# Optimization experiments

Hardware: AMD Instinct MI355X
Metric: run time of the kernel (lower is better)

The kernel has to match this reference:

```python
import jax, jax.numpy as jnp
import numpy as np

H = 128          # image resolution (matches init_kwargs H)
B = 2            # batch (matches init_kwargs B)
F = 1024         # number of triangle faces
PI = 3.141592653589793


def setup_inputs() -> dict:
    key = jax.random.key(0)
    # vertices in NDC [-1, 1]: [B, faces, 3 verts, xyz]
    v = jax.random.uniform(key, (B, F, 3, 3), dtype=jnp.float32, minval=-1.0, maxval=1.0)
    return {"v_tensor": v, "C": 16}


def _render(tmp, C):
    # tmp: [B,F,3,3] with (x,y) already in pixel coords, z in [-1,1].
    # Counting-sort rasterization expressed in closed form: instead of sorting
    # per-pixel ray/mesh intersections into in/out intervals, we use the signed
    # (winding-number) formulation: occupancy f(zt) = sum_i s_i * H(zt - zt_i)
    # where s_i = +1 for front faces, -1 for back faces. The cosine (FOF)
    # coefficients then reduce to a sum over intersections -- fully vectorized.
    x = tmp[..., 0]  # [B,F,3]
    y = tmp[..., 1]
    z = tmp[..., 2]
    px = jnp.arange(H, dtype=tmp.dtype)[None, :]   # pixel-center x, [1,H]
    py = jnp.arange(H, dtype=tmp.dtype)[:, None]   # pixel-center y, [H,1]

    def vert(i):
        return x[..., i, None, None], y[..., i, None, None], z[..., i, None, None]

    x0, y0, z0 = vert(0)
    x1, y1, z1 = vert(1)
    x2, y2, z2 = vert(2)

    # edge functions -> barycentric numerators, each [B,F,H,H]
    e0 = (x2 - x1) * (py - y1) - (y2 - y1) * (px - x1)
    e1 = (x0 - x2) * (py - y2) - (y0 - y2) * (px - x2)
    e2 = (x1 - x0) * (py - y0) - (y1 - y0) * (px - x0)
    area = (x1 - x0) * (y2 - y0) - (x2 - x0) * (y1 - y0)  # [B,F,1,1]

    nz = area != 0
    inv = jnp.where(nz, 1.0 / jnp.where(nz, area, 1.0), 0.0)
    l0, l1, l2 = e0 * inv, e1 * inv, e2 * inv
    inside = (l0 >= 0) & (l1 >= 0) & (l2 >= 0) & nz
    s = jnp.sign(area)                      # front/back facing sign
    w = jnp.where(inside, s, jnp.zeros((), tmp.dtype))  # [B,F,H,H]

    # interpolated depth, remapped to zt in [0,1]
    zt = jnp.clip((l0 * z0 + l1 * z1 + l2 * z2 + 1.0) * 0.5, 0.0, 1.0)

    # Fourier occupancy coefficients over zt in [0,1]:
    #   c0 = int f dzt           = sum_i s_i * (1 - zt_i)
    #   ck = 2 int f cos(k pi zt) dzt = -2/(k pi) * sum_i s_i * sin(k pi zt_i)
    coeffs = [jnp.sum(w * (1.0 - zt), axis=1)]            # [B,H,H]
    for k in range(1, C):
        coeffs.append(jnp.sum(w * jnp.sin((k * PI) * zt), axis=1) * (-2.0 / (k * PI)))
    return jnp.stack(coeffs, axis=1)  # [B,C,H,H]


def reference(v_tensor, C):
    a = jnp.array([H / 2.0, -H / 2.0, 1.0], dtype=v_tensor.dtype)
    b = jnp.array([H / 2.0 - 0.5, H / 2.0 - 0.5, 0.0], dtype=v_tensor.dtype)
    tmp = v_tensor * a + b  # affine transform from the torch forward
    return _render(tmp, C)
```

## Files before the change

### kernel.cpp

```cpp
#include <hip/hip_runtime.h>
#include <math.h>

#define HH 128
#define BB 2
#define FF 1024
#define CC 16
#define PIF 3.14159265358979323846f
#define RS 14

__global__ __launch_bounds__(256) void fof_setup(const float* __restrict__ v,
                                                 double* __restrict__ rec,
                                                 int* __restrict__ bbox) {
#pragma clang fp contract(off)
    int idx = blockIdx.x * 256 + threadIdx.x;
    if (idx >= BB * FF) return;
    const float* vp = v + (size_t)idx * 9;

    double X0 = fma((double)vp[0],  64.0, 63.5);
    double Y0 = fma((double)vp[1], -64.0, 63.5);
    double Z0 = (double)vp[2];
    double X1 = fma((double)vp[3],  64.0, 63.5);
    double Y1 = fma((double)vp[4], -64.0, 63.5);
    double Z1 = (double)vp[5];
    double X2 = fma((double)vp[6],  64.0, 63.5);
    double Y2 = fma((double)vp[7], -64.0, 63.5);
    double Z2 = (double)vp[8];

    double d0x = X2 - X1, d0y = Y2 - Y1;
    double d1x = X0 - X2, d1y = Y0 - Y2;
    double d2x = X1 - X0, d2y = Y1 - Y0;
    double area = d1x * d2y - d1y * d2x;
    double inv  = (area != 0.0) ? 1.0 / area : 0.0;
    double sg   = (area > 0.0) ? 1.0 : ((area < 0.0) ? -1.0 : 0.0);

    double A0 = d0x * inv, B0 = -d0y * inv, C0 = (d0y * X1 - d0x * Y1) * inv;
    double A1 = d1x * inv, B1 = -d1y * inv, C1 = (d1y * X2 - d1x * Y2) * inv;
    double A2 = d2x * inv, B2 = -d2y * inv, C2 = (d2y * X0 - d2x * Y0) * inv;

    double ZA = (A0 * Z0 + A1 * Z1 + A2 * Z2) * 0.5;
    double ZB = (B0 * Z0 + B1 * Z1 + B2 * Z2) * 0.5;
    double ZC = (C0 * Z0 + C1 * Z1 + C2 * Z2 + 1.0) * 0.5;

    double* r = rec + (size_t)idx * RS;
    r[0] = A0; r[1] = B0; r[2] = C0;
    r[3] = A1; r[4] = B1; r[5] = C1;
    r[6] = A2; r[7] = B2; r[8] = C2;
    r[9] = sg; r[10] = ZA; r[11] = ZB; r[12] = ZC; r[13] = 0.0;

    float x0 = (float)X0, y0 = (float)Y0;
    float x1 = (float)X1, y1 = (float)Y1;
    float x2 = (float)X2, y2 = (float)Y2;
    float xmn = fminf(x0, fminf(x1, x2)) - 0.5f;
    float xmx = fmaxf(x0, fmaxf(x1, x2)) + 0.5f;
    float ymn = fminf(y0, fminf(y1, y2)) - 0.5f;
    float ymx = fmaxf(y0, fmaxf(y1, y2)) + 0.5f;
    int txmin = (int)ceilf((xmn - 7.f) * 0.125f);
    int txmax = (int)floorf(xmx * 0.125f);
    int tymin = (int)ceilf((ymn - 7.f) * 0.125f);
    int tymax = (int)floorf(ymx * 0.125f);
    txmin = max(0, min(15, txmin)); txmax = max(0, min(15, txmax));
    tymin = max(0, min(15, tymin)); tymax = max(0, min(15, tymax));
    bbox[idx] = (sg == 0.0) ? (1 | (0 << 8) | (1 << 16) | (0 << 24))
                            : (txmin | (txmax << 8) | (tymin << 16) | (tymax << 24));
}

__global__ __launch_bounds__(512) void fof_main(const double* __restrict__ rec,
                                                const int* __restrict__ bbox,
                                                float* __restrict__ part) {
    __shared__ float S1[4][64][17];
    __shared__ float S2[2][64][17];
    __shared__ float S3[64][17];

    int blk  = blockIdx.x;
    int b    = blk >> 9;
    int rest = blk & 511;
    int half = rest >> 8;
    int tile = rest & 255;
    int ty   = tile >> 4;
    int tx   = tile & 15;
    int wv   = __builtin_amdgcn_readfirstlane((int)(threadIdx.x >> 6));
    int lane = threadIdx.x & 63;

    double pxd = (double)(tx * 8 + (lane & 7));
    double pyd = (double)(ty * 8 + (lane >> 3));

    float acc[CC];
#pragma unroll
    for (int k = 0; k < CC; ++k) acc[k] = 0.f;

    int gfb = b * FF + half * 512 + wv * 64;

    int pk = bbox[gfb + lane];
    int txmin = pk & 255, txmax = (pk >> 8) & 255;
    int tymin = (pk >> 16) & 255, tymax = (pk >> 24) & 255;
    bool pass = !((tx < txmin) | (tx > txmax) | (ty < tymin) | (ty > tymax));
    unsigned long long m = __ballot(pass);

    const double* rp = rec + (size_t)gfb * RS;
    while (m) {
        int j = __builtin_ctzll(m);
        m &= m - 1;
        j = __builtin_amdgcn_readfirstlane(j);
        const double* r = rp + j * RS;

        double l0 = fma(r[0], pyd, fma(r[1], pxd, r[2]));
        double l1 = fma(r[3], pyd, fma(r[4], pxd, r[5]));
        double l2 = fma(r[6], pyd, fma(r[7], pxd, r[8]));
        bool inside = (l0 >= 0.0) & (l1 >= 0.0) & (l2 >= 0.0);

        if (__any(inside)) {
            double u = fma(r[10], pyd, fma(r[11], pxd, r[12]));
            u = fmin(fmax(u, 0.0), 1.0);
            float zt = (float)u;
            float w  = inside ? (float)r[9] : 0.f;

            float t = PIF * zt;
            float s1, c1;
            __sincosf(t, &s1, &c1);
            acc[0] = fmaf(w, 1.f - zt, acc[0]);
            acc[1] = fmaf(w, s1, acc[1]);
            float twoc = c1 + c1;
            float skm2 = 0.f, skm1 = s1;
#pragma unroll
            for (int k = 2; k < CC; ++k) {
                float sk = fmaf(twoc, skm1, -skm2);
                acc[k] = fmaf(w, sk, acc[k]);
                skm2 = skm1;
                skm1 = sk;
            }
        }
    }

    if (wv >= 4) {
#pragma unroll
        for (int k = 0; k < CC; ++k) S1[wv - 4][lane][k] = acc[k];
    }
    __syncthreads();
    if (wv < 4) {
#pragma unroll
        for (int k = 0; k < CC; ++k) acc[k] += S1[wv][lane][k];
    }
    if (wv == 2 || wv == 3) {
#pragma unroll
        for (int k = 0; k < CC; ++k) S2[wv - 2][lane][k] = acc[k];
    }
    __syncthreads();
    if (wv < 2) {
#pragma unroll
        for (int k = 0; k < CC; ++k) acc[k] += S2[wv][lane][k];
    }
    if (wv == 1) {
#pragma unroll
        for (int k = 0; k < CC; ++k) S3[lane][k] = acc[k];
    }
    __syncthreads();
    if (wv == 0) {
        int xo = tx * 8 + (lane & 7);
        int yo = ty * 8 + (lane >> 3);
#pragma unroll
        for (int k = 0; k < CC; ++k) {
            part[(((b * 2 + half) * CC + k) * (HH * HH)) + yo * HH + xo] =
                acc[k] + S3[lane][k];
        }
    }
}

__global__ __launch_bounds__(256) void fof_combine(const float4* __restrict__ part4,
                                                   float4* __restrict__ out4) {
    int i   = blockIdx.x * 256 + threadIdx.x;
    int b   = i >> 16;
    int rem = i & 65535;
    int k   = rem >> 12;
    int r   = rem & 4095;
    float4 p0 = part4[(b * 32 + k) * 4096 + r];
    float4 p1 = part4[(b * 32 + 16 + k) * 4096 + r];
    float scale = (k == 0) ? 1.f : (-2.f / (PIF * (float)k));
    float4 o;
    o.x = (p0.x + p1.x) * scale;
    o.y = (p0.y + p1.y) * scale;
    o.z = (p0.z + p1.z) * scale;
    o.w = (p0.w + p1.w) * scale;
    out4[(b * 16 + k) * 4096 + r] = o;
}

extern "C" void kernel_launch(void* const* d_in, const int* in_sizes, int n_in,
                              void* d_out, int out_size, void* d_ws, size_t ws_size,
                              hipStream_t stream) {
    const float* v = (const float*)d_in[0];
    float* out = (float*)d_out;

    double* rec  = (double*)d_ws;
    int*    bbox = (int*)((char*)d_ws + 229376);
    float*  part = (float*)((char*)d_ws + 237568);

    fof_setup<<<(BB * FF + 255) / 256, 256, 0, stream>>>(v, rec, bbox);
    fof_main<<<BB * 2 * 256, 512, 0, stream>>>(rec, bbox, part);
    fof_combine<<<512, 256, 0, stream>>>((const float4*)part, (float4*)out);
}
```

Before: 85.61 us.

## Use fp32 edge tests with fp64 fallback, packed sin recurrence, drop combine kernel

The inner rasterization loop now evaluates edge functions and depth in fp32, with a per-face error bound. It falls back to the fp64 coefficients only when some lane's edge value lies within that bound, so the fp64 work is kept off the hot path. The sin harmonics use hardware v_sin/v_cos in revolution units and a two-wide packed Chebyshev recurrence. Each block now covers all 1024 faces with 1024 threads, which removes the half split and the separate combine kernel, at the cost of half as many blocks and a deeper shared-memory reduction.

```diff
diff --git a/kernel.cpp b/kernel.cpp
--- a/kernel.cpp
+++ b/kernel.cpp
@@ -6,12 +6,13 @@
 #define FF 1024
 #define CC 16
 #define PIF 3.14159265358979323846f
-#define RS 14
+
+typedef float f2 __attribute__((ext_vector_type(2)));
 
 __global__ __launch_bounds__(256) void fof_setup(const float* __restrict__ v,
-                                                 double* __restrict__ rec,
+                                                 float* __restrict__ recf,
+                                                 double* __restrict__ recd,
                                                  int* __restrict__ bbox) {
-#pragma clang fp contract(off)
     int idx = blockIdx.x * 256 + threadIdx.x;
     if (idx >= BB * FF) return;
     const float* vp = v + (size_t)idx * 9;
@@ -41,11 +42,22 @@
     double ZB = (B0 * Z0 + B1 * Z1 + B2 * Z2) * 0.5;
     double ZC = (C0 * Z0 + C1 * Z1 + C2 * Z2 + 1.0) * 0.5;
 
-    double* r = rec + (size_t)idx * RS;
-    r[0] = A0; r[1] = B0; r[2] = C0;
-    r[3] = A1; r[4] = B1; r[5] = C1;
-    r[6] = A2; r[7] = B2; r[8] = C2;
-    r[9] = sg; r[10] = ZA; r[11] = ZB; r[12] = ZC; r[13] = 0.0;
+    double M0 = (fabs(A0) + fabs(B0)) * 135.0 + fabs(C0);
+    double M1 = (fabs(A1) + fabs(B1)) * 135.0 + fabs(C1);
+    double M2 = (fabs(A2) + fabs(B2)) * 135.0 + fabs(C2);
+    float eps = (float)(1e-6 * fmax(M0, fmax(M1, M2)));
+
+    float* rf = recf + (size_t)idx * 16;
+    rf[0] = (float)A0; rf[1] = (float)B0; rf[2] = (float)C0;
+    rf[3] = (float)A1; rf[4] = (float)B1; rf[5] = (float)C1;
+    rf[6] = (float)A2; rf[7] = (float)B2; rf[8] = (float)C2;
+    rf[9] = (float)ZA; rf[10] = (float)ZB; rf[11] = (float)ZC;
+    rf[12] = (float)sg; rf[13] = eps; rf[14] = 0.f; rf[15] = 0.f;
+
+    double* rd = recd + (size_t)idx * 10;
+    rd[0] = A0; rd[1] = B0; rd[2] = C0;
+    rd[3] = A1; rd[4] = B1; rd[5] = C1;
+    rd[6] = A2; rd[7] = B2; rd[8] = C2; rd[9] = 0.0;
 
     float x0 = (float)X0, y0 = (float)Y0;
     float x1 = (float)X1, y1 = (float)Y1;
@@ -64,31 +76,32 @@
                             : (txmin | (txmax << 8) | (tymin << 16) | (tymax << 24));
 }
 
-__global__ __launch_bounds__(512) void fof_main(const double* __restrict__ rec,
-                                                const int* __restrict__ bbox,
-                                                float* __restrict__ part) {
-    __shared__ float S1[4][64][17];
-    __shared__ float S2[2][64][17];
-    __shared__ float S3[64][17];
+__global__ __launch_bounds__(1024) void fof_main(const float* __restrict__ recf,
+                                                 const double* __restrict__ recd,
+                                                 const int* __restrict__ bbox,
+                                                 float* __restrict__ out) {
+    __shared__ float S1[8][64][17];
+    __shared__ float S2[4][64][17];
+    __shared__ float S3[2][64][17];
+    __shared__ float S4[64][17];
 
     int blk  = blockIdx.x;
-    int b    = blk >> 9;
-    int rest = blk & 511;
-    int half = rest >> 8;
-    int tile = rest & 255;
+    int b    = blk >> 8;
+    int tile = blk & 255;
     int ty   = tile >> 4;
     int tx   = tile & 15;
     int wv   = __builtin_amdgcn_readfirstlane((int)(threadIdx.x >> 6));
     int lane = threadIdx.x & 63;
 
-    double pxd = (double)(tx * 8 + (lane & 7));
-    double pyd = (double)(ty * 8 + (lane >> 3));
-
-    float acc[CC];
-#pragma unroll
-    for (int k = 0; k < CC; ++k) acc[k] = 0.f;
-
-    int gfb = b * FF + half * 512 + wv * 64;
+    float px = (float)(tx * 8 + (lane & 7));
+    float py = (float)(ty * 8 + (lane >> 3));
+
+    float acc0 = 0.f, acc15 = 0.f;
+    f2 accP[7];
+#pragma unroll
+    for (int j = 0; j < 7; ++j) { accP[j].x = 0.f; accP[j].y = 0.f; }
+
+    int gfb = b * FF + wv * 64;
 
     int pk = bbox[gfb + lane];
     int txmin = pk & 255, txmax = (pk >> 8) & 255;
@@ -96,62 +109,92 @@
     bool pass = !((tx < txmin) | (tx > txmax) | (ty < tymin) | (ty > tymax));
     unsigned long long m = __ballot(pass);
 
-    const double* rp = rec + (size_t)gfb * RS;
     while (m) {
         int j = __builtin_ctzll(m);
         m &= m - 1;
         j = __builtin_amdgcn_readfirstlane(j);
-        const double* r = rp + j * RS;
-
-        double l0 = fma(r[0], pyd, fma(r[1], pxd, r[2]));
-        double l1 = fma(r[3], pyd, fma(r[4], pxd, r[5]));
-        double l2 = fma(r[6], pyd, fma(r[7], pxd, r[8]));
-        bool inside = (l0 >= 0.0) & (l1 >= 0.0) & (l2 >= 0.0);
-
-        if (__any(inside)) {
-            double u = fma(r[10], pyd, fma(r[11], pxd, r[12]));
-            u = fmin(fmax(u, 0.0), 1.0);
-            float zt = (float)u;
-            float w  = inside ? (float)r[9] : 0.f;
-
-            float t = PIF * zt;
-            float s1, c1;
-            __sincosf(t, &s1, &c1);
-            acc[0] = fmaf(w, 1.f - zt, acc[0]);
-            acc[1] = fmaf(w, s1, acc[1]);
-            float twoc = c1 + c1;
-            float skm2 = 0.f, skm1 = s1;
-#pragma unroll
-            for (int k = 2; k < CC; ++k) {
-                float sk = fmaf(twoc, skm1, -skm2);
-                acc[k] = fmaf(w, sk, acc[k]);
-                skm2 = skm1;
-                skm1 = sk;
-            }
+        const float* r = recf + (size_t)(gfb + j) * 16;
+
+        float l0 = fmaf(r[0], py, fmaf(r[1], px, r[2]));
+        float l1 = fmaf(r[3], py, fmaf(r[4], px, r[5]));
+        float l2 = fmaf(r[6], py, fmaf(r[7], px, r[8]));
+        float eps = r[13];
+        bool inside = (l0 >= 0.f) & (l1 >= 0.f) & (l2 >= 0.f);
+        bool unc = (__builtin_fabsf(l0) < eps) | (__builtin_fabsf(l1) < eps) |
+                   (__builtin_fabsf(l2) < eps);
+        if (__builtin_expect(__any(unc), 0)) {
+            const double* rd = recd + (size_t)(gfb + j) * 10;
+            double pyd = (double)py, pxd = (double)px;
+            double L0 = fma(rd[0], pyd, fma(rd[1], pxd, rd[2]));
+            double L1 = fma(rd[3], pyd, fma(rd[4], pxd, rd[5]));
+            double L2 = fma(rd[6], pyd, fma(rd[7], pxd, rd[8]));
+            inside = (L0 >= 0.0) & (L1 >= 0.0) & (L2 >= 0.0);
         }
-    }
-
-    if (wv >= 4) {
-#pragma unroll
-        for (int k = 0; k < CC; ++k) S1[wv - 4][lane][k] = acc[k];
+        float w = inside ? r[12] : 0.f;
+
+        if (__any(w != 0.f)) {
+            float zt = fmaf(r[9], py, fmaf(r[10], px, r[11]));
+            zt = fminf(fmaxf(zt, 0.f), 1.f);
+            float hz = 0.5f * zt;
+            float s1, s2, c2;
+            asm("v_sin_f32 %0, %1" : "=v"(s1) : "v"(hz));
+            asm("v_sin_f32 %0, %1" : "=v"(s2) : "v"(zt));
+            asm("v_cos_f32 %0, %1" : "=v"(c2) : "v"(zt));
+            float twoc2 = c2 + c2;
+
+            acc0 = fmaf(w, 1.f - zt, acc0);
+            f2 w2;  w2.x = w;      w2.y = w;
+            f2 t2;  t2.x = twoc2;  t2.y = twoc2;
+            f2 um1; um1.x = -s1;   um1.y = 0.f;
+            f2 u0;  u0.x = s1;     u0.y = s2;
+            accP[0] += w2 * u0;
+            f2 u1 = t2 * u0 - um1;  accP[1] += w2 * u1;
+            f2 u2 = t2 * u1 - u0;   accP[2] += w2 * u2;
+            f2 u3 = t2 * u2 - u1;   accP[3] += w2 * u3;
+            f2 u4 = t2 * u3 - u2;   accP[4] += w2 * u4;
+            f2 u5 = t2 * u4 - u3;   accP[5] += w2 * u5;
+            f2 u6 = t2 * u5 - u4;   accP[6] += w2 * u6;
+            float s15 = fmaf(twoc2, u6.x, -u5.x);
+            acc15 = fmaf(w, s15, acc15);
+        }
+    }
+
+    float accv[16];
+    accv[0] = acc0;
+#pragma unroll
+    for (int j = 0; j < 7; ++j) { accv[2 * j + 1] = accP[j].x; accv[2 * j + 2] = accP[j].y; }
+    accv[15] = acc15;
+
+    if (wv >= 8) {
+#pragma unroll
+        for (int k = 0; k < CC; ++k) S1[wv - 8][lane][k] = accv[k];
+    }
+    __syncthreads();
+    if (wv < 8) {
+#pragma unroll
+        for (int k = 0; k < CC; ++k) accv[k] += S1[wv][lane][k];
+    }
+    if (wv >= 4 && wv < 8) {
+#pragma unroll
+        for (int k = 0; k < CC; ++k) S2[wv - 4][lane][k] = accv[k];
     }
     __syncthreads();
     if (wv < 4) {
 #pragma unroll
-        for (int k = 0; k < CC; ++k) acc[k] += S1[wv][lane][k];
+        for (int k = 0; k < CC; ++k) accv[k] += S2[wv][lane][k];
     }
     if (wv == 2 || wv == 3) {
 #pragma unroll
-        for (int k = 0; k < CC; ++k) S2[wv - 2][lane][k] = acc[k];
+        for (int k = 0; k < CC; ++k) S3[wv - 2][lane][k] = accv[k];
     }
     __syncthreads();
     if (wv < 2) {
 #pragma unroll
-        for (int k = 0; k < CC; ++k) acc[k] += S2[wv][lane][k];
+        for (int k = 0; k < CC; ++k) accv[k] += S3[wv][lane][k];
     }
     if (wv == 1) {
 #pragma unroll
-        for (int k = 0; k < CC; ++k) S3[lane][k] = acc[k];
+        for (int k = 0; k < CC; ++k) S4[lane][k] = accv[k];
     }
     __syncthreads();
     if (wv == 0) {
@@ -159,28 +202,11 @@
         int yo = ty * 8 + (lane >> 3);
 #pragma unroll
         for (int k = 0; k < CC; ++k) {
-            part[(((b * 2 + half) * CC + k) * (HH * HH)) + yo * HH + xo] =
-                acc[k] + S3[lane][k];
+            float val = accv[k] + S4[lane][k];
+            float scale = (k == 0) ? 1.f : (-2.f / (PIF * (float)k));
+            out[(((b * CC + k) * HH) + yo) * HH + xo] = val * scale;
         }
     }
-}
-
-__global__ __launch_bounds__(256) void fof_combine(const float4* __restrict__ part4,
-                                                   float4* __restrict__ out4) {
-    int i   = blockIdx.x * 256 + threadIdx.x;
-    int b   = i >> 16;
-    int rem = i & 65535;
-    int k   = rem >> 12;
-    int r   = rem & 4095;
-    float4 p0 = part4[(b * 32 + k) * 4096 + r];
-    float4 p1 = part4[(b * 32 + 16 + k) * 4096 + r];
-    float scale = (k == 0) ? 1.f : (-2.f / (PIF * (float)k));
-    float4 o;
-    o.x = (p0.x + p1.x) * scale;
-    o.y = (p0.y + p1.y) * scale;
-    o.z = (p0.z + p1.z) * scale;
-    o.w = (p0.w + p1.w) * scale;
-    out4[(b * 16 + k) * 4096 + r] = o;
 }
 
 extern "C" void kernel_launch(void* const* d_in, const int* in_sizes, int n_in,
@@ -189,11 +215,10 @@
     const float* v = (const float*)d_in[0];
     float* out = (float*)d_out;
 
-    double* rec  = (double*)d_ws;
-    int*    bbox = (int*)((char*)d_ws + 229376);
-    float*  part = (float*)((char*)d_ws + 237568);
-
-    fof_setup<<<(BB * FF + 255) / 256, 256, 0, stream>>>(v, rec, bbox);
-    fof_main<<<BB * 2 * 256, 512, 0, stream>>>(rec, bbox, part);
-    fof_combine<<<512, 256, 0, stream>>>((const float4*)part, (float4*)out);
+    float*  recf = (float*)d_ws;
+    double* recd = (double*)((char*)d_ws + 131072);
+    int*    bbox = (int*)((char*)d_ws + 131072 + 163840);
+
+    fof_setup<<<(BB * FF + 255) / 256, 256, 0, stream>>>(v, recf, recd, bbox);
+    fof_main<<<BB * 256, 1024, 0, stream>>>(recf, recd, bbox, out);
 }
```

After: 81.24 us. 5.1% less time.
